# Kernel tuning notes

Measured on AMD Instinct MI355X. Metric: run time of the kernel, lower is better.

Reference implementation:

```python
import jax, jax.numpy as jnp
import numpy as np

N_PTS = 8_388_608
WIDTH, HEIGHT = 1232.0, 1616.0
K3 = jnp.array([[758.03967, 0.0, 621.46572],
                [0.0, 761.62359, 756.86402],
                [0.0, 0.0, 1.0]], dtype=jnp.float32)
MIN_D_R, MAX_D_R = 1.0, 10.0   # rewards_from_pose defaults
MIN_D_M, MAX_D_M = 1.0, 5.0    # Model pc_clip_limits
DELTA = 0.05
EPS = 1e-6


def euler_xyz(roll, pitch, yaw):
    # pytorch3d euler_angles_to_matrix(angles, 'XYZ') = Rx(roll) @ Ry(pitch) @ Rz(yaw)
    cr, sr = jnp.cos(roll), jnp.sin(roll)
    cp, sp = jnp.cos(pitch), jnp.sin(pitch)
    cy, sy = jnp.cos(yaw), jnp.sin(yaw)
    one, zero = jnp.ones_like(cr), jnp.zeros_like(cr)
    Rx = jnp.array([[one, zero, zero], [zero, cr, -sr], [zero, sr, cr]])
    Ry = jnp.array([[cp, zero, sp], [zero, one, zero], [-sp, zero, cp]])
    Rz = jnp.array([[cy, -sy, zero], [sy, cy, zero], [zero, zero, one]])
    return Rx @ Ry @ Rz


def reward_from_pose(pose, verts):
    # pose: [6] = (x, y, z, roll, pitch, yaw); verts: [N,3]
    x, y, z, roll, pitch, yaw = pose[0], pose[1], pose[2], pose[3], pose[4], pose[5]
    R = euler_xyz(roll, pitch, yaw)                 # [3,3]
    t = jnp.stack([x, y, z])                        # [3]
    v = (verts - t) @ R                             # R_inv @ p == p @ R (R orthonormal); [N,3]
    dist_mask = (v[:, 2] > MIN_D_R) & (v[:, 2] < MAX_D_R)
    p = v @ K3.T                                    # homogeneous image coords [N,3]
    u = p[:, 0] / p[:, 2]
    w = p[:, 1] / p[:, 2]
    fov_mask = (p[:, 2] > 0) & (u > 1) & (u < WIDTH - 1) & (w > 1) & (w < HEIGHT - 1)
    return jnp.sum(dist_mask & fov_mask).astype(jnp.float32)


def setup_inputs() -> dict:
    key = jax.random.key(0)
    points = 5.0 * jax.random.normal(key, (N_PTS, 3), dtype=jnp.float32)
    z0 = jnp.float32(0.0)
    return {"points": points, "x": z0, "y": z0, "z": z0,
            "roll": z0, "pitch": z0, "yaw": z0}


def reference(points, x, y, z, roll, pitch, yaw):
    pose0 = jnp.stack([x, y, z, roll, pitch, yaw])
    # 7 poses: baseline + 6 finite-difference perturbations (as in FrustumVisibilityEst.forward)
    poses = jnp.concatenate([pose0[None], pose0[None] + DELTA * jnp.eye(6, dtype=pose0.dtype)], axis=0)
    rewards = jax.vmap(reward_from_pose, in_axes=(0, None))(poses, points)  # [7]
    reward = rewards[0]
    loss = 1.0 / (reward + EPS)

    # Model.forward geometry path (uses pc_clip_limits = [1, 5])
    R = euler_xyz(roll, pitch, yaw)
    t = jnp.stack([x, y, z])
    vc = (points - t) @ R                           # camera-frame verts [N,3]
    dist_mask = (vc[:, 2] > MIN_D_M) & (vc[:, 2] < MAX_D_M)
    p = vc @ K3.T
    u = p[:, 0] / p[:, 2]
    w = p[:, 1] / p[:, 2]
    fov_mask = (p[:, 2] > 0) & (u > 1) & (u < WIDTH - 1) & (w > 1) & (w < HEIGHT - 1)
    mask = dist_mask & fov_mask
    # original does verts[mask]; we zero out masked-off rows to keep static shapes
    verts_out = jnp.where(mask[:, None], vc, jnp.zeros((), vc.dtype))
    return verts_out, loss
```

## Files before the change

kernel.cpp:

```cpp
#include <hip/hip_runtime.h>

#define N_PTS 8388608
#define FX 758.03967f
#define CXC 621.46572f
#define FY 761.62359f
#define CYC 756.86402f
#define U_MAX 1231.0f
#define W_MAX 1615.0f
#define MIN_D 1.0f
#define MAX_D_R 10.0f
#define MAX_D_M 5.0f

#define THREADS 256
#define BLOCKS 2048
#define N_UNITS (N_PTS / 4)


__global__ __launch_bounds__(256) void frustum_kernel(const float4* __restrict__ pts,
                                                      const float* __restrict__ x,
                                                      const float* __restrict__ y,
                                                      const float* __restrict__ z,
                                                      const float* __restrict__ roll,
                                                      const float* __restrict__ pitch,
                                                      const float* __restrict__ yaw,
                                                      float* __restrict__ ws,
                                                      float4* __restrict__ out) {
    __shared__ float S[12];
    if (threadIdx.x == 0) {
        float cr = cosf(*roll), sr = sinf(*roll);
        float cp = cosf(*pitch), sp = sinf(*pitch);
        float cy = cosf(*yaw),  sy = sinf(*yaw);
        S[0] = cp * cy;                S[1] = -(cp * sy);             S[2] = sp;
        S[3] = cr * sy + sr * sp * cy; S[4] = cr * cy - sr * sp * sy; S[5] = -(sr * cp);
        S[6] = sr * sy - cr * sp * cy; S[7] = sr * cy + cr * sp * sy; S[8] = cr * cp;
        S[9] = *x; S[10] = *y; S[11] = *z;
    }
    __syncthreads();

    const float R0 = S[0], R1 = S[1], R2 = S[2];
    const float R3 = S[3], R4 = S[4], R5 = S[5];
    const float R6 = S[6], R7 = S[7], R8 = S[8];
    const float t0 = S[9], t1 = S[10], t2 = S[11];

    int cnt = 0;
    auto proc = [&](float px, float py, float pz, float& ox, float& oy, float& oz) {
        float d0 = px - t0, d1 = py - t1, d2 = pz - t2;
        float v0 = fmaf(d2, R6, fmaf(d1, R3, d0 * R0));
        float v1 = fmaf(d2, R7, fmaf(d1, R4, d0 * R1));
        float v2 = fmaf(d2, R8, fmaf(d1, R5, d0 * R2));
        float p0 = fmaf(v2, CXC, v0 * FX);
        float p1 = fmaf(v2, CYC, v1 * FY);
        float u = p0 / v2;
        float w = p1 / v2;
        bool fov = (v2 > 0.0f) && (u > 1.0f) && (u < U_MAX) && (w > 1.0f) && (w < W_MAX);
        if (fov && (v2 > MIN_D) && (v2 < MAX_D_R)) cnt++;
        bool m = fov && (v2 > MIN_D) && (v2 < MAX_D_M);
        ox = m ? v0 : 0.0f;
        oy = m ? v1 : 0.0f;
        oz = m ? v2 : 0.0f;
    };

    const int stride = BLOCKS * THREADS;
    for (int unit = blockIdx.x * THREADS + threadIdx.x; unit < N_UNITS; unit += stride) {
        const long base = (long)unit * 3;
        float4 q0 = pts[base + 0];
        float4 q1 = pts[base + 1];
        float4 q2 = pts[base + 2];

        float4 o0, o1, o2;
        proc(q0.x, q0.y, q0.z, o0.x, o0.y, o0.z);
        proc(q0.w, q1.x, q1.y, o0.w, o1.x, o1.y);
        proc(q1.z, q1.w, q2.x, o1.z, o1.w, o2.x);
        proc(q2.y, q2.z, q2.w, o2.y, o2.z, o2.w);

        out[base + 0] = o0;
        out[base + 1] = o1;
        out[base + 2] = o2;
    }

    for (int off = 32; off > 0; off >>= 1) cnt += __shfl_down(cnt, off, 64);
    __shared__ int red[4];
    const int wave = threadIdx.x >> 6;
    if ((threadIdx.x & 63) == 0) red[wave] = cnt;
    __syncthreads();
    if (threadIdx.x == 0) {
        int s = red[0] + red[1] + red[2] + red[3];
        ((unsigned int*)ws)[16 + blockIdx.x] = (unsigned int)s;
    }
}

__global__ void finalize_kernel(const float* __restrict__ ws, float* __restrict__ out) {
    const unsigned int* slots = (const unsigned int*)ws + 16;
    unsigned int c = 0;
    for (int i = threadIdx.x; i < BLOCKS; i += 256) c += slots[i];
    for (int off = 32; off > 0; off >>= 1) c += __shfl_down(c, off, 64);
    __shared__ unsigned int red[4];
    const int wave = threadIdx.x >> 6;
    if ((threadIdx.x & 63) == 0) red[wave] = c;
    __syncthreads();
    if (threadIdx.x == 0) {
        unsigned int tot = red[0] + red[1] + red[2] + red[3];
        out[(long)3 * N_PTS] = 1.0f / ((float)tot + 1e-6f);
    }
}

extern "C" void kernel_launch(void* const* d_in, const int* in_sizes, int n_in,
                              void* d_out, int out_size, void* d_ws, size_t ws_size,
                              hipStream_t stream) {
    const float* points = (const float*)d_in[0];
    const float* x      = (const float*)d_in[1];
    const float* y      = (const float*)d_in[2];
    const float* z      = (const float*)d_in[3];
    const float* roll   = (const float*)d_in[4];
    const float* pitch  = (const float*)d_in[5];
    const float* yaw    = (const float*)d_in[6];
    float* ws = (float*)d_ws;
    float* out = (float*)d_out;

    frustum_kernel<<<BLOCKS, THREADS, 0, stream>>>((const float4*)points,
                                                   x, y, z, roll, pitch, yaw,
                                                   ws, (float4*)out);
    finalize_kernel<<<1, 256, 0, stream>>>(ws, out);
}
```

Baseline: 209.8 us.

## Stage points through LDS for coalesced loads and stores, one tile per block

Replaces the grid-stride loop with one 1024-point tile per block. The block loads the tile into shared memory with fully coalesced float4 accesses, lets each thread read its 12 contiguous floats from LDS, writes the results back to LDS, and stores them to global memory coalesced. The aim is to remove the 48-byte per-lane stride of the old global accesses, at the cost of LDS traffic, an extra barrier and four times as many blocks for the finalize reduction to sum.

```diff
diff --git a/kernel.cpp b/kernel.cpp
--- a/kernel.cpp
+++ b/kernel.cpp
@@ -12,8 +12,7 @@
 #define MAX_D_M 5.0f
 
 #define THREADS 256
-#define BLOCKS 2048
-#define N_UNITS (N_PTS / 4)
+#define BLOCKS (N_PTS / 1024)
 
 
 __global__ __launch_bounds__(256) void frustum_kernel(const float4* __restrict__ pts,
@@ -25,8 +24,17 @@
                                                       const float* __restrict__ yaw,
                                                       float* __restrict__ ws,
                                                       float4* __restrict__ out) {
+    __shared__ float4 st[768];
     __shared__ float S[12];
-    if (threadIdx.x == 0) {
+
+    const int t = threadIdx.x;
+    const long gbase = (long)blockIdx.x * 768;
+
+    st[t]       = pts[gbase + t];
+    st[t + 256] = pts[gbase + t + 256];
+    st[t + 512] = pts[gbase + t + 512];
+
+    if (t == 0) {
         float cr = cosf(*roll), sr = sinf(*roll);
         float cp = cosf(*pitch), sp = sinf(*pitch);
         float cy = cosf(*yaw),  sy = sinf(*yaw);
@@ -41,6 +49,11 @@
     const float R3 = S[3], R4 = S[4], R5 = S[5];
     const float R6 = S[6], R7 = S[7], R8 = S[8];
     const float t0 = S[9], t1 = S[10], t2 = S[11];
+
+    const float4* pv = (const float4*)((const float*)st + t * 12);
+    float4 q0 = pv[0];
+    float4 q1 = pv[1];
+    float4 q2 = pv[2];
 
     int cnt = 0;
     auto proc = [&](float px, float py, float pz, float& ox, float& oy, float& oz) {
@@ -60,23 +73,21 @@
         oz = m ? v2 : 0.0f;
     };
 
-    const int stride = BLOCKS * THREADS;
-    for (int unit = blockIdx.x * THREADS + threadIdx.x; unit < N_UNITS; unit += stride) {
-        const long base = (long)unit * 3;
-        float4 q0 = pts[base + 0];
-        float4 q1 = pts[base + 1];
-        float4 q2 = pts[base + 2];
+    float4 o0, o1, o2;
+    proc(q0.x, q0.y, q0.z, o0.x, o0.y, o0.z);
+    proc(q0.w, q1.x, q1.y, o0.w, o1.x, o1.y);
+    proc(q1.z, q1.w, q2.x, o1.z, o1.w, o2.x);
+    proc(q2.y, q2.z, q2.w, o2.y, o2.z, o2.w);
 
-        float4 o0, o1, o2;
-        proc(q0.x, q0.y, q0.z, o0.x, o0.y, o0.z);
-        proc(q0.w, q1.x, q1.y, o0.w, o1.x, o1.y);
-        proc(q1.z, q1.w, q2.x, o1.z, o1.w, o2.x);
-        proc(q2.y, q2.z, q2.w, o2.y, o2.z, o2.w);
+    float4* wv = (float4*)((float*)st + t * 12);
+    wv[0] = o0;
+    wv[1] = o1;
+    wv[2] = o2;
+    __syncthreads();
 
-        out[base + 0] = o0;
-        out[base + 1] = o1;
-        out[base + 2] = o2;
-    }
+    out[gbase + t]       = st[t];
+    out[gbase + t + 256] = st[t + 256];
+    out[gbase + t + 512] = st[t + 512];
 
     for (int off = 32; off > 0; off >>= 1) cnt += __shfl_down(cnt, off, 64);
     __shared__ int red[4];
@@ -84,8 +95,8 @@
     if ((threadIdx.x & 63) == 0) red[wave] = cnt;
     __syncthreads();
     if (threadIdx.x == 0) {
-        int s = red[0] + red[1] + red[2] + red[3];
-        ((unsigned int*)ws)[16 + blockIdx.x] = (unsigned int)s;
+        ((unsigned int*)ws)[16 + blockIdx.x] =
+            (unsigned int)(red[0] + red[1] + red[2] + red[3]);
     }
 }
 
```

After: 196.7 us. 1.07x faster.
